# Kernel optimization log

Measured on AMD Instinct MI355X. Metric: run time of the kernel, lower is better.

## Reference

```python
import jax, jax.numpy as jnp
import numpy as np
from jax import lax

EPS = 1e-07
PATCH = 3  # patch_size -> padding = 1 with 1x1 kernels
PROP = 3   # propagate_size -> 3x3 sum pool (avg_pool*9)


def setup_inputs() -> dict:
    key = jax.random.key(0)
    k1, k2 = jax.random.split(key)
    foreground = jax.random.normal(k1, (4, 128, 64, 64), dtype=jnp.float32)
    mask = jax.random.uniform(k2, (4, 1, 64, 64), dtype=jnp.float32)
    return {"foreground": foreground, "mask": mask}


def _cattention_single(x, m):
    # x: (c, h, w); m: (1, h, w)
    c, h, w = x.shape
    pad = PATCH // 2  # = 1
    # dynamic 1x1 conv kernels: (h*w, c), one kernel per spatial location
    k = x.reshape(c, h * w).T + EPS
    k = k / jnp.sqrt(jnp.sum(k * k, axis=1, keepdims=True))
    # F.conv2d(x, k, padding=1) with 1x1 kernels -> zero-pad then matmul
    x_pad = jnp.pad(x, ((0, 0), (pad, pad), (pad, pad)))  # (c, h+2, w+2)
    scores = jnp.einsum('lc,cij->lij', k, x_pad)  # (hw, h+2, w+2)
    # avg_pool2d(3,1,padding=1) * 9 == 3x3 sum pool with zero padding
    scores = lax.reduce_window(scores, 0.0, lax.add,
                               window_dimensions=(1, 3, 3),
                               window_strides=(1, 1, 1),
                               padding=((0, 0), (1, 1), (1, 1)))
    att = jax.nn.softmax(scores, axis=0)  # softmax over the hw channel dim
    # conv_transpose2d with 1x1 kernels, padding=1 -> crop border then matmul
    att_c = att[:, pad:-pad, pad:-pad]  # (hw, h, w)
    recovered = jnp.einsum('lij,lc->cij', att_c, k)  # (c, h, w)
    recovered = recovered * (1.0 - m) / float(PATCH ** 2)
    return recovered + x * m


def reference(foreground, mask):
    return jax.vmap(_cattention_single)(foreground, mask)
```

## Files before the change

### kernel.cpp

```cpp
#include <hip/hip_runtime.h>


typedef short bf16x8 __attribute__((ext_vector_type(8)));
typedef float f32x4 __attribute__((ext_vector_type(4)));
typedef unsigned short u16x4 __attribute__((ext_vector_type(4)));
typedef unsigned int u32x2 __attribute__((ext_vector_type(2)));

#define L2E 1.4426950408889634f

__device__ __forceinline__ unsigned short f2bf(float f) {
    unsigned int u;
    __builtin_memcpy(&u, &f, 4);
    u = u + 0x7FFFu + ((u >> 16) & 1u);
    return (unsigned short)(u >> 16);
}
__device__ __forceinline__ float bf2f(unsigned short h) {
    unsigned int u = ((unsigned int)h) << 16;
    float f;
    __builtin_memcpy(&f, &u, 4);
    return f;
}
__device__ __forceinline__ unsigned int pk_bf16(float a, float b) {
    unsigned int ua, ub;
    __builtin_memcpy(&ua, &a, 4);
    __builtin_memcpy(&ub, &b, 4);
    return ((ua + 0x8000u) >> 16) | ((ub + 0x8000u) & 0xFFFF0000u);
}
__device__ __forceinline__ void gl_lds16(const unsigned short* g, unsigned short* l) {
    __builtin_amdgcn_global_load_lds(
        (const __attribute__((address_space(1))) unsigned int*)g,
        (__attribute__((address_space(3))) unsigned int*)l, 16, 0, 0);
}

__global__ void prep_inv(const float* __restrict__ x, float* __restrict__ inv) {
    const int b = blockIdx.y, l0 = blockIdx.x * 64, t = threadIdx.x;
    const int wave = t >> 6, lane = t & 63;
    const float* xb = x + (size_t)b * 128 * 4096 + l0 + lane;
    float sq = 0.f;
#pragma unroll
    for (int i = 0; i < 32; i++) {
        float v = xb[(size_t)(wave * 32 + i) * 4096] + 1e-7f;
        sq += v * v;
    }
    __shared__ float sqp[256];
    sqp[t] = sq;
    __syncthreads();
    if (t < 64)
        inv[b * 4096 + l0 + t] = rsqrtf(sqp[t] + sqp[64 + t] + sqp[128 + t] + sqp[192 + t]);
}

__global__ void prep_main(const float* __restrict__ x,
                          const float* __restrict__ inv,
                          unsigned short* __restrict__ kmat,
                          unsigned short* __restrict__ kT,
                          unsigned short* __restrict__ xbT) {
    const int p = blockIdx.x, b = blockIdx.y, cb = blockIdx.z * 64;
    const int t = threadIdx.x, wave = t >> 6, lane = t & 63;

    __shared__ float sX[8][3][66];
    __shared__ float sMidT[64 * 68];
    __shared__ __align__(16) unsigned short sQ[64 * 80];
    __shared__ float sInv[64];
    if (t < 64) sInv[t] = inv[b * 4096 + p * 64 + t];

    for (int c0 = 0; c0 < 64; c0 += 8) {
        __syncthreads();
#pragma unroll
        for (int i = 0; i < 6; i++) {
            int pair = wave * 6 + i;
            int cc = pair / 3, r = pair - cc * 3;
            int pp = p + r - 1;
            float v = 0.f;
            if ((unsigned)pp < 64u)
                v = x[((size_t)b * 128 + cb + c0 + cc) * 4096 + pp * 64 + lane];
            sX[cc][r][1 + lane] = v;
        }
        if (t < 48) {
            int cc = t / 6, rr = (t % 6) >> 1, side = t & 1;
            sX[cc][rr][side * 65] = 0.f;
        }
        __syncthreads();
#pragma unroll
        for (int j = 0; j < 2; j++) {
            int cc = wave * 2 + j;
            float mid = sX[cc][1][1 + lane] + 1e-7f;
            sMidT[lane * 68 + c0 + cc] = mid;
            float sbox = 0.f;
#pragma unroll
            for (int r = 0; r < 3; r++)
                sbox += sX[cc][r][lane] + sX[cc][r][lane + 1] + sX[cc][r][lane + 2];
            sQ[lane * 80 + c0 + cc] = f2bf(sbox * L2E);
        }
    }
    __syncthreads();

#pragma unroll
    for (int i = 0; i < 2; i++) {
        int u = i * 256 + t, row = u >> 3, g = u & 7;
        *(bf16x8*)(xbT + ((size_t)b * 4096 + p * 64 + row) * 128 + cb + g * 8) =
            *(const bf16x8*)(sQ + row * 80 + g * 8);
    }
#pragma unroll
    for (int i = 0; i < 2; i++) {
        int u = i * 256 + t, q = u >> 3, g = u & 7;
        float iv = sInv[q];
        f32x4 a = *(const f32x4*)(sMidT + q * 68 + g * 8);
        f32x4 c = *(const f32x4*)(sMidT + q * 68 + g * 8 + 4);
        unsigned int w[4];
        w[0] = pk_bf16(a[0] * iv, a[1] * iv);
        w[1] = pk_bf16(a[2] * iv, a[3] * iv);
        w[2] = pk_bf16(c[0] * iv, c[1] * iv);
        w[3] = pk_bf16(c[2] * iv, c[3] * iv);
        int Gs = ((int)blockIdx.z * 8 + g) ^ (q & 15);
        *(uint4*)(kmat + ((size_t)b * 4096 + p * 64 + q) * 128 + Gs * 8) =
            make_uint4(w[0], w[1], w[2], w[3]);
    }
    {
        int cl = t >> 2, qg = t & 3;
        unsigned int w[8];
#pragma unroll
        for (int j = 0; j < 8; j++) {
            int ql = qg * 16 + j * 2;
            w[j] = pk_bf16(sMidT[ql * 68 + cl] * sInv[ql],
                           sMidT[(ql + 1) * 68 + cl] * sInv[ql + 1]);
        }
        unsigned short* dst = kT + ((size_t)b * 128 + cb + cl) * 4096 + p * 64;
        int h0 = (qg * 2) ^ (cl & 7), h1 = (qg * 2 + 1) ^ (cl & 7);
        *(uint4*)(dst + h0 * 8) = make_uint4(w[0], w[1], w[2], w[3]);
        *(uint4*)(dst + h1 * 8) = make_uint4(w[4], w[5], w[6], w[7]);
    }
}

#define SP_STRIDE 72
#define SK_REGION 9216
#define SV_OFF 9216
#define SMEM_ELEMS (SK_REGION + 8192)

__global__ void __launch_bounds__(256, 3) flash_attn(
        const unsigned short* __restrict__ kmat,
        const unsigned short* __restrict__ kT,
        const unsigned short* __restrict__ xbT,
        unsigned short* __restrict__ opart,
        float* __restrict__ lsum,
        int nsplit, int qbshift) {
    const int combo = blockIdx.x & (4 * nsplit - 1);
    const int qb = blockIdx.x >> qbshift;
    const int b = combo & 3, split = combo >> 2;
    const int nk = 4096 / nsplit, NIT = nk >> 6, kt_base = split * nk;
    const int t = threadIdx.x;
    const int wave = t >> 6, lane = t & 63;
    const int l16 = lane & 15, quad = lane >> 4;

    __shared__ __align__(16) unsigned short smem[SMEM_ELEMS];
    unsigned short* sK = smem;
    unsigned short* sV = smem + SV_OFF;
    unsigned short* sP = smem + wave * 32 * SP_STRIDE;

    bf16x8 aq[2][4];
#pragma unroll
    for (int h = 0; h < 2; h++) {
        const unsigned short* xq =
            xbT + ((size_t)b * 4096 + qb * 128 + wave * 32 + h * 16 + l16) * 128 + quad * 8;
#pragma unroll
        for (int cc = 0; cc < 4; cc++) aq[h][cc] = *(const bf16x8*)(xq + cc * 32);
    }

    f32x4 o[2][8];
#pragma unroll
    for (int h = 0; h < 2; h++)
#pragma unroll
        for (int n = 0; n < 8; n++) o[h][n] = (f32x4){0.f, 0.f, 0.f, 0.f};
    float rs[2] = {0.f, 0.f};

    const unsigned short* kmb = kmat + (size_t)b * 4096 * 128;
    const unsigned short* ktb = kT + (size_t)b * 128 * 4096;

    for (int it = 0; it < NIT; it++) {
        const int kt0 = kt_base + it * 64;
        __syncthreads();
        {
            const unsigned short* gK = kmb + (size_t)kt0 * 128;
#pragma unroll
            for (int i = 0; i < 4; i++) {
                int e = i * 2048 + t * 8;
                gl_lds16(gK + e, sK + i * 2048 + wave * 512);
                gl_lds16(ktb + (size_t)(e >> 6) * 4096 + kt0 + (e & 63),
                         sV + i * 2048 + wave * 512);
            }
        }
        __syncthreads();

        f32x4 s[2][4];
#pragma unroll
        for (int h = 0; h < 2; h++)
#pragma unroll
            for (int k4 = 0; k4 < 4; k4++) s[h][k4] = (f32x4){0.f, 0.f, 0.f, 0.f};
#pragma unroll
        for (int cc = 0; cc < 4; cc++) {
#pragma unroll
            for (int k4 = 0; k4 < 4; k4++) {
                bf16x8 ak = *(const bf16x8*)(sK + (k4 * 16 + l16) * 128 +
                                             (((cc * 4 + quad) ^ l16) * 8));
                s[0][k4] = __builtin_amdgcn_mfma_f32_16x16x32_bf16(ak, aq[0][cc], s[0][k4], 0, 0, 0);
                s[1][k4] = __builtin_amdgcn_mfma_f32_16x16x32_bf16(ak, aq[1][cc], s[1][k4], 0, 0, 0);
            }
        }
        __syncthreads();

#pragma unroll
        for (int h = 0; h < 2; h++) {
#pragma unroll
            for (int k4 = 0; k4 < 4; k4++) {
                float p0 = exp2f(s[h][k4][0]), p1 = exp2f(s[h][k4][1]);
                float p2 = exp2f(s[h][k4][2]), p3 = exp2f(s[h][k4][3]);
                rs[h] += (p0 + p1) + (p2 + p3);
                u32x2 d;
                d[0] = pk_bf16(p0, p1);
                d[1] = pk_bf16(p2, p3);
                *(u32x2*)(sP + (h * 16 + l16) * SP_STRIDE + k4 * 16 + quad * 4) = d;
            }
        }
        asm volatile("" ::: "memory");
        bf16x8 pa[2][2];
#pragma unroll
        for (int h = 0; h < 2; h++)
#pragma unroll
            for (int kc = 0; kc < 2; kc++)
                pa[h][kc] = *(const bf16x8*)(sP + (h * 16 + l16) * SP_STRIDE + kc * 32 + quad * 8);
        asm volatile("" ::: "memory");

#pragma unroll
        for (int kc = 0; kc < 2; kc++)
#pragma unroll
            for (int n = 0; n < 8; n++) {
                bf16x8 bv = *(const bf16x8*)(sV + (n * 16 + l16) * 64 +
                                             (((kc * 4 + quad) ^ (l16 & 7)) * 8));
                o[0][n] = __builtin_amdgcn_mfma_f32_16x16x32_bf16(pa[0][kc], bv, o[0][n], 0, 0, 0);
                o[1][n] = __builtin_amdgcn_mfma_f32_16x16x32_bf16(pa[1][kc], bv, o[1][n], 0, 0, 0);
            }
    }

#pragma unroll
    for (int h = 0; h < 2; h++) {
        rs[h] += __shfl_xor(rs[h], 16);
        rs[h] += __shfl_xor(rs[h], 32);
    }
    if (lane < 16) {
#pragma unroll
        for (int h = 0; h < 2; h++)
            lsum[(size_t)(split * 4 + b) * 4096 + qb * 128 + wave * 32 + h * 16 + lane] = rs[h];
    }

    __syncthreads();
    unsigned short* sO = smem;
    unsigned int* sO32 = (unsigned int*)smem;
#pragma unroll
    for (int h = 0; h < 2; h++)
#pragma unroll
        for (int n = 0; n < 8; n++) {
            int c = n * 16 + l16;
            int q = wave * 32 + h * 16 + quad * 4;
            sO32[(c * 136 + q) >> 1] = pk_bf16(o[h][n][0], o[h][n][1]);
            sO32[(c * 136 + q + 2) >> 1] = pk_bf16(o[h][n][2], o[h][n][3]);
        }
    __syncthreads();
#pragma unroll
    for (int i = 0; i < 8; i++) {
        int u = i * 256 + t, c = u >> 4, chunk = u & 15;
        *(uint4*)(opart + ((size_t)(split * 4 + b) * 128 + c) * 4096 + qb * 128 + chunk * 8) =
            *(const uint4*)(sO + c * 136 + chunk * 8);
    }
}

__global__ void combine(const unsigned short* __restrict__ opart,
                        const float* __restrict__ lsum,
                        const float* __restrict__ x,
                        const float* __restrict__ mask,
                        float* __restrict__ out, int S) {
    const int qb = blockIdx.x, b = blockIdx.y, t = threadIdx.x;
    __shared__ float Linv[64];
    if (t < 64) {
        float L = 0.f;
        for (int s2 = 0; s2 < S; s2++)
            L += lsum[(size_t)(s2 * 4 + b) * 4096 + qb * 64 + t];
        Linv[t] = 1.f / fmaxf(L, 1e-37f);
    }
    __syncthreads();
#pragma unroll
    for (int i = 0; i < 8; i++) {
        int c = (t >> 4) + i * 16, qj = (t & 15) * 4;
        size_t qoff = (size_t)qb * 64 + qj;
        f32x4 acc = (f32x4){0.f, 0.f, 0.f, 0.f};
        for (int s2 = 0; s2 < S; s2++) {
            u16x4 pv = *(const u16x4*)(opart + ((size_t)(s2 * 4 + b) * 128 + c) * 4096 + qoff);
#pragma unroll
            for (int j = 0; j < 4; j++) acc[j] += bf2f(pv[j]);
        }
        f32x4 xv = *(const f32x4*)(x + ((size_t)b * 128 + c) * 4096 + qoff);
        f32x4 mv = *(const f32x4*)(mask + (size_t)b * 4096 + qoff);
        f32x4 res;
#pragma unroll
        for (int j = 0; j < 4; j++)
            res[j] = acc[j] * Linv[qj + j] * (1.f - mv[j]) * (1.f / 9.f) + xv[j] * mv[j];
        *(f32x4*)(out + ((size_t)b * 128 + c) * 4096 + qoff) = res;
    }
}

extern "C" void kernel_launch(void* const* d_in, const int* in_sizes, int n_in,
                              void* d_out, int out_size, void* d_ws, size_t ws_size,
                              hipStream_t stream) {
    const float* x = (const float*)d_in[0];
    const float* mask = (const float*)d_in[1];
    float* out = (float*)d_out;
    char* ws = (char*)d_ws;
    unsigned short* kmat = (unsigned short*)(ws);
    unsigned short* kT   = (unsigned short*)(ws + (size_t)4 * 1024 * 1024);
    unsigned short* xbT  = (unsigned short*)(ws + (size_t)8 * 1024 * 1024);
    float* lsum          = (float*)(ws + (size_t)12 * 1024 * 1024);
    float* inv           = (float*)(ws + (size_t)12 * 1024 * 1024 + 512 * 1024);
    unsigned short* opart = (unsigned short*)(ws + (size_t)13 * 1024 * 1024);

    int S, qbshift;
    if (ws_size >= (size_t)45 * 1024 * 1024)      { S = 8; qbshift = 5; }
    else if (ws_size >= (size_t)29 * 1024 * 1024) { S = 4; qbshift = 4; }
    else if (ws_size >= (size_t)21 * 1024 * 1024) { S = 2; qbshift = 3; }
    else return;

    prep_inv<<<dim3(64, 4), 256, 0, stream>>>(x, inv);
    prep_main<<<dim3(64, 4, 2), 256, 0, stream>>>(x, inv, kmat, kT, xbT);
    flash_attn<<<dim3(32 * 4 * S), 256, 0, stream>>>(kmat, kT, xbT, opart, lsum, S, qbshift);
    combine<<<dim3(64, 4), 256, 0, stream>>>(opart, lsum, x, mask, out, S);
}
```

Measured before the change: 176.2 us.

## Double-buffer K/V tiles in flash kernel, fuse prep kernels, cap split at 4

The flash attention loop now double-buffers the K and V tiles in LDS, issuing async global-to-LDS loads for the next tile while the softmax and PV stages of the current tile run. This doubles LDS use, so launch bounds drop to 2 blocks per CU. The two prep kernels are merged into one that computes the inverse norms in-block over all 128 channels, removing a launch and the inv buffer but halving prep's grid. The key split is capped at 4, giving fewer flash blocks and a smaller combine.

Result: faster. 159.5 us (-9.5%).

```diff
diff --git a/kernel.cpp b/kernel.cpp
--- a/kernel.cpp
+++ b/kernel.cpp
@@ -32,38 +32,21 @@
         (__attribute__((address_space(3))) unsigned int*)l, 16, 0, 0);
 }
 
-__global__ void prep_inv(const float* __restrict__ x, float* __restrict__ inv) {
-    const int b = blockIdx.y, l0 = blockIdx.x * 64, t = threadIdx.x;
-    const int wave = t >> 6, lane = t & 63;
-    const float* xb = x + (size_t)b * 128 * 4096 + l0 + lane;
-    float sq = 0.f;
-#pragma unroll
-    for (int i = 0; i < 32; i++) {
-        float v = xb[(size_t)(wave * 32 + i) * 4096] + 1e-7f;
-        sq += v * v;
-    }
+__global__ void prep(const float* __restrict__ x,
+                     unsigned short* __restrict__ kmat,
+                     unsigned short* __restrict__ kT,
+                     unsigned short* __restrict__ xbT) {
+    const int p = blockIdx.x, b = blockIdx.y;
+    const int t = threadIdx.x, wave = t >> 6, lane = t & 63;
+
+    __shared__ float sX[8][3][66];
+    __shared__ float sMidT[64 * 132];
+    __shared__ __align__(16) unsigned short sQ[64 * 136];
     __shared__ float sqp[256];
-    sqp[t] = sq;
-    __syncthreads();
-    if (t < 64)
-        inv[b * 4096 + l0 + t] = rsqrtf(sqp[t] + sqp[64 + t] + sqp[128 + t] + sqp[192 + t]);
-}
-
-__global__ void prep_main(const float* __restrict__ x,
-                          const float* __restrict__ inv,
-                          unsigned short* __restrict__ kmat,
-                          unsigned short* __restrict__ kT,
-                          unsigned short* __restrict__ xbT) {
-    const int p = blockIdx.x, b = blockIdx.y, cb = blockIdx.z * 64;
-    const int t = threadIdx.x, wave = t >> 6, lane = t & 63;
-
-    __shared__ float sX[8][3][66];
-    __shared__ float sMidT[64 * 68];
-    __shared__ __align__(16) unsigned short sQ[64 * 80];
     __shared__ float sInv[64];
-    if (t < 64) sInv[t] = inv[b * 4096 + p * 64 + t];
-
-    for (int c0 = 0; c0 < 64; c0 += 8) {
+
+    float sqacc = 0.f;
+    for (int c0 = 0; c0 < 128; c0 += 8) {
         __syncthreads();
 #pragma unroll
         for (int i = 0; i < 6; i++) {
@@ -72,7 +55,7 @@
             int pp = p + r - 1;
             float v = 0.f;
             if ((unsigned)pp < 64u)
-                v = x[((size_t)b * 128 + cb + c0 + cc) * 4096 + pp * 64 + lane];
+                v = x[((size_t)b * 128 + c0 + cc) * 4096 + pp * 64 + lane];
             sX[cc][r][1 + lane] = v;
         }
         if (t < 48) {
@@ -84,47 +67,53 @@
         for (int j = 0; j < 2; j++) {
             int cc = wave * 2 + j;
             float mid = sX[cc][1][1 + lane] + 1e-7f;
-            sMidT[lane * 68 + c0 + cc] = mid;
+            sMidT[lane * 132 + c0 + cc] = mid;
+            sqacc += mid * mid;
             float sbox = 0.f;
 #pragma unroll
             for (int r = 0; r < 3; r++)
                 sbox += sX[cc][r][lane] + sX[cc][r][lane + 1] + sX[cc][r][lane + 2];
-            sQ[lane * 80 + c0 + cc] = f2bf(sbox * L2E);
-        }
-    }
-    __syncthreads();
-
-#pragma unroll
-    for (int i = 0; i < 2; i++) {
-        int u = i * 256 + t, row = u >> 3, g = u & 7;
-        *(bf16x8*)(xbT + ((size_t)b * 4096 + p * 64 + row) * 128 + cb + g * 8) =
-            *(const bf16x8*)(sQ + row * 80 + g * 8);
-    }
-#pragma unroll
-    for (int i = 0; i < 2; i++) {
-        int u = i * 256 + t, q = u >> 3, g = u & 7;
+            sQ[lane * 136 + c0 + cc] = f2bf(sbox * L2E);
+        }
+    }
+    sqp[t] = sqacc;
+    __syncthreads();
+    if (t < 64)
+        sInv[t] = rsqrtf(sqp[t] + sqp[64 + t] + sqp[128 + t] + sqp[192 + t]);
+    __syncthreads();
+
+#pragma unroll
+    for (int i = 0; i < 4; i++) {
+        int u = i * 256 + t, row = u >> 4, g = u & 15;
+        *(bf16x8*)(xbT + ((size_t)b * 4096 + p * 64 + row) * 128 + g * 8) =
+            *(const bf16x8*)(sQ + row * 136 + g * 8);
+    }
+#pragma unroll
+    for (int i = 0; i < 4; i++) {
+        int u = i * 256 + t, q = u >> 4, G = u & 15;
         float iv = sInv[q];
-        f32x4 a = *(const f32x4*)(sMidT + q * 68 + g * 8);
-        f32x4 c = *(const f32x4*)(sMidT + q * 68 + g * 8 + 4);
+        f32x4 a = *(const f32x4*)(sMidT + q * 132 + G * 8);
+        f32x4 c = *(const f32x4*)(sMidT + q * 132 + G * 8 + 4);
         unsigned int w[4];
         w[0] = pk_bf16(a[0] * iv, a[1] * iv);
         w[1] = pk_bf16(a[2] * iv, a[3] * iv);
         w[2] = pk_bf16(c[0] * iv, c[1] * iv);
         w[3] = pk_bf16(c[2] * iv, c[3] * iv);
-        int Gs = ((int)blockIdx.z * 8 + g) ^ (q & 15);
+        int Gs = G ^ (q & 15);
         *(uint4*)(kmat + ((size_t)b * 4096 + p * 64 + q) * 128 + Gs * 8) =
             make_uint4(w[0], w[1], w[2], w[3]);
     }
-    {
-        int cl = t >> 2, qg = t & 3;
+#pragma unroll
+    for (int i = 0; i < 2; i++) {
+        int u = i * 256 + t, cl = u >> 2, qg = u & 3;
         unsigned int w[8];
 #pragma unroll
         for (int j = 0; j < 8; j++) {
             int ql = qg * 16 + j * 2;
-            w[j] = pk_bf16(sMidT[ql * 68 + cl] * sInv[ql],
-                           sMidT[(ql + 1) * 68 + cl] * sInv[ql + 1]);
-        }
-        unsigned short* dst = kT + ((size_t)b * 128 + cb + cl) * 4096 + p * 64;
+            w[j] = pk_bf16(sMidT[ql * 132 + cl] * sInv[ql],
+                           sMidT[(ql + 1) * 132 + cl] * sInv[ql + 1]);
+        }
+        unsigned short* dst = kT + ((size_t)b * 128 + cl) * 4096 + p * 64;
         int h0 = (qg * 2) ^ (cl & 7), h1 = (qg * 2 + 1) ^ (cl & 7);
         *(uint4*)(dst + h0 * 8) = make_uint4(w[0], w[1], w[2], w[3]);
         *(uint4*)(dst + h1 * 8) = make_uint4(w[4], w[5], w[6], w[7]);
@@ -132,11 +121,10 @@
 }
 
 #define SP_STRIDE 72
-#define SK_REGION 9216
-#define SV_OFF 9216
-#define SMEM_ELEMS (SK_REGION + 8192)
-
-__global__ void __launch_bounds__(256, 3) flash_attn(
+#define BUF_STRIDE 17408
+#define SMEM_ELEMS (2 * BUF_STRIDE)
+
+__global__ void __launch_bounds__(256, 2) flash_attn(
         const unsigned short* __restrict__ kmat,
         const unsigned short* __restrict__ kT,
         const unsigned short* __restrict__ xbT,
@@ -152,9 +140,6 @@
     const int l16 = lane & 15, quad = lane >> 4;
 
     __shared__ __align__(16) unsigned short smem[SMEM_ELEMS];
-    unsigned short* sK = smem;
-    unsigned short* sV = smem + SV_OFF;
-    unsigned short* sP = smem + wave * 32 * SP_STRIDE;
 
     bf16x8 aq[2][4];
 #pragma unroll
@@ -175,19 +160,23 @@
     const unsigned short* kmb = kmat + (size_t)b * 4096 * 128;
     const unsigned short* ktb = kT + (size_t)b * 128 * 4096;
 
+    {
+        const unsigned short* gK = kmb + (size_t)kt_base * 128;
+#pragma unroll
+        for (int i = 0; i < 4; i++) {
+            int e = i * 2048 + t * 8;
+            gl_lds16(gK + e, smem + i * 2048 + wave * 512);
+            gl_lds16(ktb + (size_t)(e >> 6) * 4096 + kt_base + (e & 63),
+                     smem + 9216 + i * 2048 + wave * 512);
+        }
+    }
+
     for (int it = 0; it < NIT; it++) {
-        const int kt0 = kt_base + it * 64;
-        __syncthreads();
-        {
-            const unsigned short* gK = kmb + (size_t)kt0 * 128;
-#pragma unroll
-            for (int i = 0; i < 4; i++) {
-                int e = i * 2048 + t * 8;
-                gl_lds16(gK + e, sK + i * 2048 + wave * 512);
-                gl_lds16(ktb + (size_t)(e >> 6) * 4096 + kt0 + (e & 63),
-                         sV + i * 2048 + wave * 512);
-            }
-        }
+        const int base = (it & 1) * BUF_STRIDE;
+        unsigned short* sK = smem + base;
+        unsigned short* sV = smem + base + 9216;
+        unsigned short* sP = sK + wave * 32 * SP_STRIDE;
+
         __syncthreads();
 
         f32x4 s[2][4];
@@ -206,6 +195,19 @@
             }
         }
         __syncthreads();
+
+        if (it + 1 < NIT) {
+            const int kt0 = kt_base + (it + 1) * 64;
+            unsigned short* nb = smem + ((it + 1) & 1) * BUF_STRIDE;
+            const unsigned short* gK = kmb + (size_t)kt0 * 128;
+#pragma unroll
+            for (int i = 0; i < 4; i++) {
+                int e = i * 2048 + t * 8;
+                gl_lds16(gK + e, nb + i * 2048 + wave * 512);
+                gl_lds16(ktb + (size_t)(e >> 6) * 4096 + kt0 + (e & 63),
+                         nb + 9216 + i * 2048 + wave * 512);
+            }
+        }
 
 #pragma unroll
         for (int h = 0; h < 2; h++) {
@@ -317,17 +319,14 @@
     unsigned short* kT   = (unsigned short*)(ws + (size_t)4 * 1024 * 1024);
     unsigned short* xbT  = (unsigned short*)(ws + (size_t)8 * 1024 * 1024);
     float* lsum          = (float*)(ws + (size_t)12 * 1024 * 1024);
-    float* inv           = (float*)(ws + (size_t)12 * 1024 * 1024 + 512 * 1024);
     unsigned short* opart = (unsigned short*)(ws + (size_t)13 * 1024 * 1024);
 
     int S, qbshift;
-    if (ws_size >= (size_t)45 * 1024 * 1024)      { S = 8; qbshift = 5; }
-    else if (ws_size >= (size_t)29 * 1024 * 1024) { S = 4; qbshift = 4; }
+    if (ws_size >= (size_t)29 * 1024 * 1024)      { S = 4; qbshift = 4; }
     else if (ws_size >= (size_t)21 * 1024 * 1024) { S = 2; qbshift = 3; }
     else return;
 
-    prep_inv<<<dim3(64, 4), 256, 0, stream>>>(x, inv);
-    prep_main<<<dim3(64, 4, 2), 256, 0, stream>>>(x, inv, kmat, kT, xbT);
+    prep<<<dim3(64, 4), 256, 0, stream>>>(x, kmat, kT, xbT);
     flash_attn<<<dim3(32 * 4 * S), 256, 0, stream>>>(kmat, kT, xbT, opart, lsum, S, qbshift);
     combine<<<dim3(64, 4), 256, 0, stream>>>(opart, lsum, x, mask, out, S);
 }
```
